# Kernel tuning notes

Hardware: AMD Instinct MI355X
Metric: run time of the kernel (lower is better)

The kernel has to match this reference:

```python
import jax, jax.numpy as jnp
import numpy as np

N_NODES = 30000
N_EDGES = 300000
NUM_GRAPHS = 512
HID = 600
IN_FEATS = 9
NUM_TASKS = 128


def setup_inputs() -> dict:
    key = jax.random.key(0)
    ks = jax.random.split(key, 20)
    s = 0.05  # small init scale to keep activations bounded over 5 layers
    inp = {
        'x': jax.random.normal(ks[0], (N_NODES, IN_FEATS), jnp.float32),
        'edge_index': jax.random.randint(ks[1], (2, N_EDGES), 0, N_NODES, jnp.int64),
        'batch_ind': jnp.sort(jax.random.randint(ks[2], (N_NODES,), 0, NUM_GRAPHS, jnp.int64)),
        'w1_0': jax.random.normal(ks[3], (IN_FEATS, HID), jnp.float32) * s,
        'b1_0': jax.random.normal(ks[4], (HID,), jnp.float32) * s,
        'w2_0': jax.random.normal(ks[5], (HID, HID), jnp.float32) * s,
        'b2_0': jax.random.normal(ks[6], (HID,), jnp.float32) * s,
        'w1_r': jax.random.normal(ks[7], (4, HID, HID), jnp.float32) * s,
        'b1_r': jax.random.normal(ks[8], (4, HID), jnp.float32) * s,
        'w2_r': jax.random.normal(ks[9], (4, HID, HID), jnp.float32) * s,
        'b2_r': jax.random.normal(ks[10], (4, HID), jnp.float32) * s,
        'cw1': jax.random.normal(ks[11], (HID, 256), jnp.float32) * s,
        'cb1': jax.random.normal(ks[12], (256,), jnp.float32) * s,
        'cw2': jax.random.normal(ks[13], (256, 256), jnp.float32) * s,
        'cb2': jax.random.normal(ks[14], (256,), jnp.float32) * s,
        'cw3': jax.random.normal(ks[15], (256, NUM_TASKS), jnp.float32) * s,
        'cb3': jax.random.normal(ks[16], (NUM_TASKS,), jnp.float32) * s,
    }
    return inp


def _gin_conv(h, edge_index, w1, b1, w2, b2):
    # sum-aggregate neighbor features: messages flow src -> dst
    msgs = h[edge_index[0]]                                   # [E, d] gather
    agg = jax.ops.segment_sum(msgs, edge_index[1], num_segments=N_NODES)
    z = h + agg                                               # (1 + eps) * x + agg, eps = 0
    z = jax.nn.relu(z @ w1 + b1) @ w2 + b2                    # per-layer MLP [in, 600, 600]
    return z


def _forward(x, edge_index, batch_ind, w1_0, b1_0, w2_0, b2_0,
             w1_r, b1_r, w2_r, b2_r, cw1, cb1, cw2, cb2, cw3, cb3):
    h = _gin_conv(x, edge_index, w1_0, b1_0, w2_0, b2_0)
    h = jax.nn.relu(h)  # inter-layer activation (dropout is identity in eval)
    for i in range(4):  # layers 1..4 (fixed, structurally distinct params)
        h = _gin_conv(h, edge_index, w1_r[i], b1_r[i], w2_r[i], b2_r[i])
        if i < 3:
            h = jax.nn.relu(h)  # no act/dropout after final GNN layer (jk=None)
    feats = jax.ops.segment_sum(h, batch_ind, num_segments=NUM_GRAPHS)  # global_add_pool
    z = jax.nn.relu(feats @ cw1 + cb1)
    z = jax.nn.relu(z @ cw2 + cb2)
    return z @ cw3 + cb3  # [NUM_GRAPHS, NUM_TASKS]


def reference(x, edge_index, batch_ind, w1_0, b1_0, w2_0, b2_0,
              w1_r, b1_r, w2_r, b2_r, cw1, cb1, cw2, cb2, cw3, cb3):
    return _forward(x, edge_index, batch_ind, w1_0, b1_0, w2_0, b2_0,
                    w1_r, b1_r, w2_r, b2_r, cw1, cb1, cw2, cb2, cw3, cb3)
```

## Files before the change

### kernel.cpp

```cpp
#include <hip/hip_runtime.h>

#define N_NODES 30000
#define N_EDGES 300000
#define NUM_GRAPHS 512
#define HID 600
#define IN_FEATS 9
#define NUM_TASKS 128

#define MPAD 30080
#define HPAD 640
#define K0PAD 32

typedef __attribute__((ext_vector_type(4))) float f32x4;
typedef __attribute__((ext_vector_type(8))) short bf16x8;


__device__ __forceinline__ float bflo(unsigned int v) {
  union { unsigned int u; float f; } c; c.u = v << 16; return c.f;
}
__device__ __forceinline__ float bfhi(unsigned int v) {
  union { unsigned int u; float f; } c; c.u = v & 0xffff0000u; return c.f;
}
__device__ __forceinline__ unsigned short f2bf(float f) {
  union { float f; unsigned int u; } c; c.f = f;
  unsigned int u = c.u;
  return (unsigned short)((u + 0x7fffu + ((u >> 16) & 1u)) >> 16);
}
__device__ __forceinline__ unsigned int pack2(float a, float b) {
  return (unsigned int)f2bf(a) | ((unsigned int)f2bf(b) << 16);
}


__global__ void k_hist(const int* __restrict__ keys, int* __restrict__ counts, int n) {
  int i = blockIdx.x * blockDim.x + threadIdx.x;
  if (i < n) atomicAdd(&counts[keys[i]], 1);
}

__global__ __launch_bounds__(1024) void k_exscan(const int* __restrict__ in,
                                                 int* __restrict__ out,
                                                 int* cursor, int n) {
  __shared__ int buf[1024];
  int tid = threadIdx.x;
  int CH = (n + 1023) / 1024;
  int base = tid * CH;
  int s = 0;
  for (int j = 0; j < CH; ++j) {
    int i = base + j;
    if (i < n) s += in[i];
  }
  buf[tid] = s;
  __syncthreads();
  for (int off = 1; off < 1024; off <<= 1) {
    int t = (tid >= off) ? buf[tid - off] : 0;
    __syncthreads();
    buf[tid] += t;
    __syncthreads();
  }
  int pre = (tid == 0) ? 0 : buf[tid - 1];
  for (int j = 0; j < CH; ++j) {
    int i = base + j;
    if (i <= n) out[i] = pre;
    if (i < n) {
      int v = in[i];
      if (cursor) cursor[i] = pre;
      pre += v;
    }
  }
}

__global__ __launch_bounds__(256) void k_scan1(const int* __restrict__ in,
                                               int* __restrict__ partials, int n) {
  __shared__ int buf[256];
  int i = blockIdx.x * 256 + threadIdx.x;
  buf[threadIdx.x] = (i < n) ? in[i] : 0;
  __syncthreads();
  for (int off = 128; off; off >>= 1) {
    if (threadIdx.x < off) buf[threadIdx.x] += buf[threadIdx.x + off];
    __syncthreads();
  }
  if (threadIdx.x == 0) partials[blockIdx.x] = buf[0];
}

__global__ __launch_bounds__(256) void k_scan3(const int* __restrict__ in,
                                               const int* __restrict__ poff,
                                               int* __restrict__ out,
                                               int* __restrict__ cursor, int n) {
  __shared__ int buf[256];
  int b = blockIdx.x, t = threadIdx.x;
  int i = b * 256 + t;
  int v = (i < n) ? in[i] : 0;
  buf[t] = v;
  __syncthreads();
  for (int off = 1; off < 256; off <<= 1) {
    int x = (t >= off) ? buf[t - off] : 0;
    __syncthreads();
    buf[t] += x;
    __syncthreads();
  }
  int base = poff[b];
  int excl = base + buf[t] - v;
  if (i < n) {
    out[i] = excl;
    cursor[i] = excl;
    if (i == n - 1) out[n] = base + buf[t];
  }
}

__global__ void k_scatter(const int* __restrict__ src, const int* __restrict__ dst,
                          int* __restrict__ cursor, int* __restrict__ edge_src, int E) {
  int e = blockIdx.x * blockDim.x + threadIdx.x;
  if (e < E) {
    int pos = atomicAdd(&cursor[dst[e]], 1);
    edge_src[pos] = src[e];
  }
}


__global__ void k_wt0(const float* __restrict__ w1_0, unsigned short* __restrict__ wt0) {
  int idx = blockIdx.x * 256 + threadIdx.x;
  if (idx >= HPAD * K0PAD) return;
  int n = idx / K0PAD, k = idx % K0PAD;
  float v = (n < HID && k < IN_FEATS) ? w1_0[(size_t)k * HID + n] : 0.f;
  wt0[idx] = f2bf(v);
}

__global__ __launch_bounds__(256) void k_wt_tiled(
    const float* __restrict__ w2_0, const float* __restrict__ w1_r,
    const float* __restrict__ w2_r, unsigned short* __restrict__ wts) {
  __shared__ float tile[64][65];
  int b = blockIdx.x;
  int w = b / 100;
  int tb = b % 100;
  int tn = (tb % 10) * 64;
  int tk = (tb / 10) * 64;
  const float* W;
  if (w == 0) W = w2_0;
  else if (w < 5) W = w1_r + (size_t)(w - 1) * HID * HID;
  else W = w2_r + (size_t)(w - 5) * HID * HID;
  int t = threadIdx.x;
  int lx = t & 63, ly = t >> 6;
#pragma unroll
  for (int i = 0; i < 16; ++i) {
    int k = tk + ly + i * 4;
    int n = tn + lx;
    float v = (k < HID && n < HID) ? W[(size_t)k * HID + n] : 0.f;
    tile[ly + i * 4][lx] = v;
  }
  __syncthreads();
  unsigned short* dst = wts + (size_t)w * HPAD * HPAD;
#pragma unroll
  for (int i = 0; i < 16; ++i) {
    int n = tn + ly + i * 4;
    int k = tk + lx;
    dst[(size_t)n * HPAD + k] = f2bf(tile[lx][ly + i * 4]);
  }
}

__global__ void k_bias_all(const float* __restrict__ b1_0, const float* __restrict__ b2_0,
                           const float* __restrict__ b1_r, const float* __restrict__ b2_r,
                           float* __restrict__ biases) {
  int idx = blockIdx.x * 256 + threadIdx.x;
  if (idx >= 10 * HPAD) return;
  int w = idx / HPAD, i = idx % HPAD;
  float v = 0.f;
  if (i < HID) {
    if (w == 0) v = b1_0[i];
    else if (w == 1) v = b2_0[i];
    else if (w < 6) v = b1_r[(size_t)(w - 2) * HID + i];
    else v = b2_r[(size_t)(w - 6) * HID + i];
  }
  biases[idx] = v;
}

__global__ void k_xconv(const float* __restrict__ x, unsigned short* __restrict__ xb) {
  int idx = blockIdx.x * 256 + threadIdx.x;
  if (idx >= MPAD * K0PAD) return;
  int m = idx >> 5, k = idx & 31;
  float v = (m < N_NODES && k < IN_FEATS) ? x[(size_t)m * IN_FEATS + k] : 0.f;
  xb[idx] = f2bf(v);
}


template <int U>
__global__ __launch_bounds__(256) void k_agg_bf16(
    const unsigned int* __restrict__ h, const int* __restrict__ ptr,
    const int* __restrict__ esrc, unsigned int* __restrict__ z, int n_nodes) {
  int wave = threadIdx.x >> 6, lane = threadIdx.x & 63;
  int node = blockIdx.x * 4 + wave;
  if (node >= n_nodes) return;
  int beg = ptr[node], end = ptr[node + 1];
  const unsigned int* hn = h + (size_t)node * U;
  float a0[5], a1[5];
#pragma unroll
  for (int i = 0; i < 5; ++i) {
    int u = lane + i * 64;
    if (u < U) { unsigned int v = hn[u]; a0[i] = bflo(v); a1[i] = bfhi(v); }
    else { a0[i] = 0.f; a1[i] = 0.f; }
  }
  int e = beg;
  for (; e + 4 <= end; e += 4) {
    const unsigned int* p0 = h + (size_t)esrc[e] * U;
    const unsigned int* p1 = h + (size_t)esrc[e + 1] * U;
    const unsigned int* p2 = h + (size_t)esrc[e + 2] * U;
    const unsigned int* p3 = h + (size_t)esrc[e + 3] * U;
    unsigned int v0[5], v1[5], v2[5], v3[5];
#pragma unroll
    for (int i = 0; i < 5; ++i) {
      int u = lane + i * 64;
      if (u < U) { v0[i] = p0[u]; v1[i] = p1[u]; v2[i] = p2[u]; v3[i] = p3[u]; }
      else { v0[i] = 0; v1[i] = 0; v2[i] = 0; v3[i] = 0; }
    }
#pragma unroll
    for (int i = 0; i < 5; ++i) {
      a0[i] += (bflo(v0[i]) + bflo(v1[i])) + (bflo(v2[i]) + bflo(v3[i]));
      a1[i] += (bfhi(v0[i]) + bfhi(v1[i])) + (bfhi(v2[i]) + bfhi(v3[i]));
    }
  }
  for (; e < end; ++e) {
    const unsigned int* p0 = h + (size_t)esrc[e] * U;
#pragma unroll
    for (int i = 0; i < 5; ++i) {
      int u = lane + i * 64;
      if (u < U) { unsigned int v = p0[u]; a0[i] += bflo(v); a1[i] += bfhi(v); }
    }
  }
  unsigned int* zn = z + (size_t)node * U;
#pragma unroll
  for (int i = 0; i < 5; ++i) {
    int u = lane + i * 64;
    if (u < U) zn[u] = pack2(a0[i], a1[i]);
  }
}


__global__ __launch_bounds__(256) void k_pool_bf16(
    const unsigned int* __restrict__ h, const int* __restrict__ gptr,
    float* __restrict__ feats) {
  const int U = HPAD / 2;
  __shared__ float red[4][HPAD];
  int t = threadIdx.x;
  int wave = t >> 6, lane = t & 63;
  int g = blockIdx.x;
  int beg = gptr[g], end = gptr[g + 1];
  float a0[5] = {0.f, 0.f, 0.f, 0.f, 0.f}, a1[5] = {0.f, 0.f, 0.f, 0.f, 0.f};
  for (int i = beg + wave; i < end; i += 4) {
    const unsigned int* hi = h + (size_t)i * U;
#pragma unroll
    for (int j = 0; j < 5; ++j) {
      unsigned int v = hi[lane + j * 64];
      a0[j] += bflo(v); a1[j] += bfhi(v);
    }
  }
#pragma unroll
  for (int j = 0; j < 5; ++j) {
    int u = lane + j * 64;
    red[wave][2 * u] = a0[j];
    red[wave][2 * u + 1] = a1[j];
  }
  __syncthreads();
  float* fg = feats + (size_t)g * HPAD;
  for (int c = t; c < HPAD; c += 256)
    fg[c] = red[0][c] + red[1][c] + red[2][c] + red[3][c];
}


#define GLOAD(gptr, lptr)                                                            \
  __builtin_amdgcn_global_load_lds(                                                  \
      (const __attribute__((address_space(1))) unsigned int*)(gptr),                 \
      (__attribute__((address_space(3))) unsigned int*)(lptr), 16, 0, 0)

__global__ __launch_bounds__(512, 6) void k_mgemm(
    const unsigned short* __restrict__ A, const unsigned short* __restrict__ Bt,
    const float* __restrict__ bias, unsigned short* __restrict__ C,
    int lda, int ldb, int ldc, int K, int relu, int gy) {
  int G = gridDim.x;
  int orig = blockIdx.x;
  int q = G >> 3, r = G & 7;
  int xcd = orig & 7, local = orig >> 3;
  int wgid = (xcd < r ? xcd * (q + 1) : r * (q + 1) + (xcd - r) * q) + local;
  int n0 = (wgid % gy) * 128;
  int m0 = (wgid / gy) * 128;

  __shared__ unsigned short smem[3 * 4096 * 2];
  unsigned short* Asb = smem;
  unsigned short* Bsb = smem + 12288;

  int t = threadIdx.x;
  int lane = t & 63, wave = t >> 6;
  int wm = (wave >> 2) * 64;
  int wn = (wave & 3) * 32;

  f32x4 acc[4][2] = {};

  int off = t * 8;
  int rm = off >> 5, rk = off & 31;

  const unsigned short* Ar = A + (size_t)(m0 + rm) * lda + rk;
  const unsigned short* Br = Bt + (size_t)(n0 + rm) * ldb + rk;

  int nt = K >> 5;
  GLOAD(Ar, Asb + off);
  GLOAD(Br, Bsb + off);
  if (nt > 1) {
    GLOAD(Ar + 32, Asb + 4096 + off);
    GLOAD(Br + 32, Bsb + 4096 + off);
  }

  int kk = (lane >> 4) * 8;
  int ra = wm + (lane & 15);
  int rb = wn + (lane & 15);
  int cur = 0;

  for (int tt = 0; tt < nt; ++tt) {
    if (tt + 1 < nt) {
      asm volatile("s_waitcnt vmcnt(2)" ::: "memory");
    } else {
      asm volatile("s_waitcnt vmcnt(0)" ::: "memory");
    }
    __builtin_amdgcn_s_barrier();
    if (tt + 2 < nt) {
      int k2 = (tt + 2) << 5;
      int nb = cur + 2; if (nb >= 3) nb -= 3;
      GLOAD(Ar + k2, Asb + nb * 4096 + off);
      GLOAD(Br + k2, Bsb + nb * 4096 + off);
    }
    bf16x8 a[4], b[2];
#pragma unroll
    for (int i = 0; i < 4; ++i)
      a[i] = *(const bf16x8*)(Asb + cur * 4096 + (ra + i * 16) * 32 + kk);
#pragma unroll
    for (int j = 0; j < 2; ++j)
      b[j] = *(const bf16x8*)(Bsb + cur * 4096 + (rb + j * 16) * 32 + kk);
#pragma unroll
    for (int i = 0; i < 4; ++i)
#pragma unroll
      for (int j = 0; j < 2; ++j)
        acc[i][j] = __builtin_amdgcn_mfma_f32_16x16x32_bf16(b[j], a[i], acc[i][j], 0, 0, 0);
    cur += 1; if (cur >= 3) cur = 0;
  }

  __syncthreads();
  int colm = lane & 15;
  int nq = (lane >> 4) * 4;
#pragma unroll
  for (int j = 0; j < 2; ++j) {
    int nloc = wn + j * 16 + nq;
    f32x4 bv = *(const f32x4*)&bias[n0 + nloc];
#pragma unroll
    for (int i = 0; i < 4; ++i) {
      int mloc = wm + i * 16 + colm;
      float v0 = acc[i][j][0] + bv[0];
      float v1 = acc[i][j][1] + bv[1];
      float v2 = acc[i][j][2] + bv[2];
      float v3 = acc[i][j][3] + bv[3];
      if (relu) {
        v0 = fmaxf(v0, 0.f); v1 = fmaxf(v1, 0.f);
        v2 = fmaxf(v2, 0.f); v3 = fmaxf(v3, 0.f);
      }
      uint2 w;
      w.x = pack2(v0, v1);
      w.y = pack2(v2, v3);
      int nblk = (nloc >> 2) ^ ((mloc & 7) << 2);
      *(uint2*)&smem[mloc * 128 + nblk * 4] = w;
    }
  }
  __syncthreads();
#pragma unroll
  for (int p = 0; p < 4; ++p) {
    int idx = p * 4096 + t * 8;
    int mloc = idx >> 7;
    int ncol = idx & 127;
    int s = (mloc & 7) << 2;
    int nb0 = (ncol >> 2) ^ s;
    int nb1 = ((ncol >> 2) + 1) ^ s;
    uint2 w0 = *(uint2*)&smem[mloc * 128 + nb0 * 4];
    uint2 w1 = *(uint2*)&smem[mloc * 128 + nb1 * 4];
    uint4 w;
    w.x = w0.x; w.y = w0.y; w.z = w1.x; w.w = w1.y;
    *(uint4*)&C[(size_t)(m0 + mloc) * ldc + n0 + ncol] = w;
  }
}


__global__ __launch_bounds__(256) void k_classifier(
    const float* __restrict__ feats,
    const float* __restrict__ cw1, const float* __restrict__ cb1,
    const float* __restrict__ cw2, const float* __restrict__ cb2,
    const float* __restrict__ cw3, const float* __restrict__ cb3,
    float* __restrict__ out) {
  __shared__ float f[HID];
  __shared__ float red[4][256];
  __shared__ float z1[256];
  __shared__ float z2[256];
  int g = blockIdx.x;
  int t = threadIdx.x;
  int wave = t >> 6, lane = t & 63;
  for (int i = t; i < HID; i += 256) f[i] = feats[(size_t)g * HPAD + i];
  __syncthreads();

  {
    float acc[4] = {0.f, 0.f, 0.f, 0.f};
    int k0 = wave * 150, k1 = k0 + 150;
    for (int k = k0; k < k1; ++k) {
      float fv = f[k];
      const float* row = cw1 + (size_t)k * 256;
#pragma unroll
      for (int j = 0; j < 4; ++j) acc[j] += fv * row[lane + j * 64];
    }
#pragma unroll
    for (int j = 0; j < 4; ++j) red[wave][lane + j * 64] = acc[j];
  }
  __syncthreads();
  z1[t] = fmaxf(red[0][t] + red[1][t] + red[2][t] + red[3][t] + cb1[t], 0.f);
  __syncthreads();

  {
    float acc[4] = {0.f, 0.f, 0.f, 0.f};
    int k0 = wave * 64, k1 = k0 + 64;
    for (int k = k0; k < k1; ++k) {
      float zv = z1[k];
      const float* row = cw2 + (size_t)k * 256;
#pragma unroll
      for (int j = 0; j < 4; ++j) acc[j] += zv * row[lane + j * 64];
    }
    __syncthreads();
#pragma unroll
    for (int j = 0; j < 4; ++j) red[wave][lane + j * 64] = acc[j];
  }
  __syncthreads();
  z2[t] = fmaxf(red[0][t] + red[1][t] + red[2][t] + red[3][t] + cb2[t], 0.f);
  __syncthreads();

  {
    float a0 = 0.f, a1 = 0.f;
    int k0 = wave * 64, k1 = k0 + 64;
    for (int k = k0; k < k1; ++k) {
      float zv = z2[k];
      const float* row = cw3 + (size_t)k * NUM_TASKS;
      a0 += zv * row[lane];
      a1 += zv * row[lane + 64];
    }
    __syncthreads();
    red[wave][lane] = a0;
    red[wave][lane + 64] = a1;
  }
  __syncthreads();
  if (t < NUM_TASKS)
    out[(size_t)g * NUM_TASKS + t] = red[0][t] + red[1][t] + red[2][t] + red[3][t] + cb3[t];
}


extern "C" void kernel_launch(void* const* d_in, const int* in_sizes, int n_in,
                              void* d_out, int out_size, void* d_ws, size_t ws_size,
                              hipStream_t stream) {
  const float* x      = (const float*)d_in[0];
  const int*   ei     = (const int*)d_in[1];
  const int*   batch  = (const int*)d_in[2];
  const float* w1_0   = (const float*)d_in[3];
  const float* b1_0   = (const float*)d_in[4];
  const float* w2_0   = (const float*)d_in[5];
  const float* b2_0   = (const float*)d_in[6];
  const float* w1_r   = (const float*)d_in[7];
  const float* b1_r   = (const float*)d_in[8];
  const float* w2_r   = (const float*)d_in[9];
  const float* b2_r   = (const float*)d_in[10];
  const float* cw1    = (const float*)d_in[11];
  const float* cb1    = (const float*)d_in[12];
  const float* cw2    = (const float*)d_in[13];
  const float* cb2    = (const float*)d_in[14];
  const float* cw3    = (const float*)d_in[15];
  const float* cb3    = (const float*)d_in[16];
  float* out = (float*)d_out;

  const int* e_src = ei;
  const int* e_dst = ei + N_EDGES;

  const size_t HBUF = (size_t)MPAD * HPAD;
  const size_t ZBUF = (size_t)MPAD * K0PAD;
  const size_t WT   = (size_t)HPAD * HPAD;
  const int NB = (N_NODES + 255) / 256;

  unsigned short* hA  = (unsigned short*)d_ws;
  unsigned short* hB  = hA + HBUF;
  unsigned short* hC  = hB + HBUF;
  unsigned short* z0  = hC + HBUF;
  unsigned short* xb  = z0 + ZBUF;
  unsigned short* wt0 = xb + ZBUF;
  unsigned short* wts = wt0 + (size_t)HPAD * K0PAD;
  float* biases = (float*)(wts + 9 * WT);
  float* feats  = biases + 10 * HPAD;
  int* row_ptr  = (int*)(feats + (size_t)NUM_GRAPHS * HPAD);
  int* counts   = row_ptr + (N_NODES + 1);
  int* edge_src = counts + N_NODES;
  int* gptr     = edge_src + N_EDGES;
  int* gcnt     = gptr + (NUM_GRAPHS + 1);
  int* partials = gcnt + NUM_GRAPHS;
  int* poff     = partials + (NB + 1);

  k_wt0<<<(HPAD * K0PAD + 255) / 256, 256, 0, stream>>>(w1_0, wt0);
  k_wt_tiled<<<9 * 100, 256, 0, stream>>>(w2_0, w1_r, w2_r, wts);
  k_bias_all<<<(10 * HPAD + 255) / 256, 256, 0, stream>>>(b1_0, b2_0, b1_r, b2_r, biases);
  k_xconv<<<(MPAD * K0PAD + 255) / 256, 256, 0, stream>>>(x, xb);

  hipMemsetAsync(counts, 0, N_NODES * sizeof(int), stream);
  k_hist<<<(N_EDGES + 255) / 256, 256, 0, stream>>>(e_dst, counts, N_EDGES);
  k_scan1<<<NB, 256, 0, stream>>>(counts, partials, N_NODES);
  k_exscan<<<1, 1024, 0, stream>>>(partials, poff, nullptr, NB);
  k_scan3<<<NB, 256, 0, stream>>>(counts, poff, row_ptr, counts, N_NODES);
  k_scatter<<<(N_EDGES + 255) / 256, 256, 0, stream>>>(e_src, e_dst, counts, edge_src, N_EDGES);

  hipMemsetAsync(gcnt, 0, NUM_GRAPHS * sizeof(int), stream);
  k_hist<<<(N_NODES + 255) / 256, 256, 0, stream>>>(batch, gcnt, N_NODES);
  k_exscan<<<1, 1024, 0, stream>>>(gcnt, gptr, nullptr, NUM_GRAPHS);

  const int G = (MPAD / 128) * (HPAD / 128);
  const int GY = HPAD / 128;

  k_agg_bf16<K0PAD / 2><<<(N_NODES + 3) / 4, 256, 0, stream>>>(
      (const unsigned int*)xb, row_ptr, edge_src, (unsigned int*)z0, N_NODES);
  k_mgemm<<<G, 512, 0, stream>>>(z0, wt0, biases + 0 * HPAD, hC, K0PAD, K0PAD, HPAD, K0PAD, 1, GY);
  k_mgemm<<<G, 512, 0, stream>>>(hC, wts, biases + 1 * HPAD, hA, HPAD, HPAD, HPAD, HPAD, 1, GY);

  unsigned short* h = hA;
  unsigned short* z = hB;
  unsigned short* tb = hC;
  for (int i = 0; i < 4; ++i) {
    k_agg_bf16<HPAD / 2><<<(N_NODES + 3) / 4, 256, 0, stream>>>(
        (const unsigned int*)h, row_ptr, edge_src, (unsigned int*)z, N_NODES);
    k_mgemm<<<G, 512, 0, stream>>>(z, wts + (1 + (size_t)i) * WT, biases + (2 + i) * HPAD, tb,
                                   HPAD, HPAD, HPAD, HPAD, 1, GY);
    k_mgemm<<<G, 512, 0, stream>>>(tb, wts + (5 + (size_t)i) * WT, biases + (6 + i) * HPAD, z,
                                   HPAD, HPAD, HPAD, HPAD, (i < 3) ? 1 : 0, GY);
    unsigned short* tmp = h; h = z; z = tmp;
  }

  k_pool_bf16<<<NUM_GRAPHS, 256, 0, stream>>>((const unsigned int*)h, gptr, feats);
  k_classifier<<<NUM_GRAPHS, 256, 0, stream>>>(feats, cw1, cb1, cw2, cb2, cw3, cb3, out);
}
```

Measured before the change: 720.9 us.

## Fuse setup kernels, merge pool with classifier, add LDS swizzle GEMM variant

Several small preprocessing kernels (weight transpose for layer 0, bias packing, x conversion, both histograms) are merged into one launch. Pooling is folded into the classifier kernel, which removes the feats buffer round trip. A templated GEMM adds an XOR swizzle on the LDS k-offset to reduce bank conflicts, but it is only used for the last two layers, which looks like an A/B experiment. MPAD also grows to 30208, adding a little padded work in exchange for launch and memory-traffic savings.

```diff
diff --git a/kernel.cpp b/kernel.cpp
--- a/kernel.cpp
+++ b/kernel.cpp
@@ -7,7 +7,7 @@
 #define IN_FEATS 9
 #define NUM_TASKS 128
 
-#define MPAD 30080
+#define MPAD 30208
 #define HPAD 640
 #define K0PAD 32
 
@@ -31,10 +31,56 @@
 }
 
 
-__global__ void k_hist(const int* __restrict__ keys, int* __restrict__ counts, int n) {
-  int i = blockIdx.x * blockDim.x + threadIdx.x;
-  if (i < n) atomicAdd(&counts[keys[i]], 1);
-}
+__global__ void k_setup(const float* __restrict__ w1_0,
+                        const float* __restrict__ b1_0, const float* __restrict__ b2_0,
+                        const float* __restrict__ b1_r, const float* __restrict__ b2_r,
+                        const float* __restrict__ x,
+                        const int* __restrict__ e_dst, const int* __restrict__ batch,
+                        unsigned short* __restrict__ wt0, float* __restrict__ biases,
+                        unsigned short* __restrict__ xb,
+                        int* __restrict__ counts, int* __restrict__ gcnt) {
+  const int S0 = HPAD * K0PAD;
+  const int S1 = 10 * HPAD;
+  const int S2 = MPAD * K0PAD;
+  const int S3 = N_EDGES;
+  int idx = blockIdx.x * 256 + threadIdx.x;
+  if (idx < S0) {
+    int n = idx / K0PAD, k = idx % K0PAD;
+    float v = (n < HID && k < IN_FEATS) ? w1_0[(size_t)k * HID + n] : 0.f;
+    wt0[idx] = f2bf(v);
+    return;
+  }
+  idx -= S0;
+  if (idx < S1) {
+    int w = idx / HPAD, i = idx % HPAD;
+    float v = 0.f;
+    if (i < HID) {
+      if (w == 0) v = b1_0[i];
+      else if (w == 1) v = b2_0[i];
+      else if (w < 6) v = b1_r[(size_t)(w - 2) * HID + i];
+      else v = b2_r[(size_t)(w - 6) * HID + i];
+    }
+    biases[idx] = v;
+    return;
+  }
+  idx -= S1;
+  if (idx < S2) {
+    int m = idx >> 5, k = idx & 31;
+    float v = (m < N_NODES && k < IN_FEATS) ? x[(size_t)m * IN_FEATS + k] : 0.f;
+    xb[idx] = f2bf(v);
+    return;
+  }
+  idx -= S2;
+  if (idx < S3) {
+    atomicAdd(&counts[e_dst[idx]], 1);
+    return;
+  }
+  idx -= S3;
+  if (idx < N_NODES) {
+    atomicAdd(&gcnt[batch[idx]], 1);
+  }
+}
+
 
 __global__ __launch_bounds__(1024) void k_exscan(const int* __restrict__ in,
                                                  int* __restrict__ out,
@@ -115,14 +161,6 @@
   }
 }
 
-
-__global__ void k_wt0(const float* __restrict__ w1_0, unsigned short* __restrict__ wt0) {
-  int idx = blockIdx.x * 256 + threadIdx.x;
-  if (idx >= HPAD * K0PAD) return;
-  int n = idx / K0PAD, k = idx % K0PAD;
-  float v = (n < HID && k < IN_FEATS) ? w1_0[(size_t)k * HID + n] : 0.f;
-  wt0[idx] = f2bf(v);
-}
 
 __global__ __launch_bounds__(256) void k_wt_tiled(
     const float* __restrict__ w2_0, const float* __restrict__ w1_r,
@@ -156,30 +194,6 @@
   }
 }
 
-__global__ void k_bias_all(const float* __restrict__ b1_0, const float* __restrict__ b2_0,
-                           const float* __restrict__ b1_r, const float* __restrict__ b2_r,
-                           float* __restrict__ biases) {
-  int idx = blockIdx.x * 256 + threadIdx.x;
-  if (idx >= 10 * HPAD) return;
-  int w = idx / HPAD, i = idx % HPAD;
-  float v = 0.f;
-  if (i < HID) {
-    if (w == 0) v = b1_0[i];
-    else if (w == 1) v = b2_0[i];
-    else if (w < 6) v = b1_r[(size_t)(w - 2) * HID + i];
-    else v = b2_r[(size_t)(w - 6) * HID + i];
-  }
-  biases[idx] = v;
-}
-
-__global__ void k_xconv(const float* __restrict__ x, unsigned short* __restrict__ xb) {
-  int idx = blockIdx.x * 256 + threadIdx.x;
-  if (idx >= MPAD * K0PAD) return;
-  int m = idx >> 5, k = idx & 31;
-  float v = (m < N_NODES && k < IN_FEATS) ? x[(size_t)m * IN_FEATS + k] : 0.f;
-  xb[idx] = f2bf(v);
-}
-
 
 template <int U>
 __global__ __launch_bounds__(256) void k_agg_bf16(
@@ -233,43 +247,13 @@
 }
 
 
-__global__ __launch_bounds__(256) void k_pool_bf16(
-    const unsigned int* __restrict__ h, const int* __restrict__ gptr,
-    float* __restrict__ feats) {
-  const int U = HPAD / 2;
-  __shared__ float red[4][HPAD];
-  int t = threadIdx.x;
-  int wave = t >> 6, lane = t & 63;
-  int g = blockIdx.x;
-  int beg = gptr[g], end = gptr[g + 1];
-  float a0[5] = {0.f, 0.f, 0.f, 0.f, 0.f}, a1[5] = {0.f, 0.f, 0.f, 0.f, 0.f};
-  for (int i = beg + wave; i < end; i += 4) {
-    const unsigned int* hi = h + (size_t)i * U;
-#pragma unroll
-    for (int j = 0; j < 5; ++j) {
-      unsigned int v = hi[lane + j * 64];
-      a0[j] += bflo(v); a1[j] += bfhi(v);
-    }
-  }
-#pragma unroll
-  for (int j = 0; j < 5; ++j) {
-    int u = lane + j * 64;
-    red[wave][2 * u] = a0[j];
-    red[wave][2 * u + 1] = a1[j];
-  }
-  __syncthreads();
-  float* fg = feats + (size_t)g * HPAD;
-  for (int c = t; c < HPAD; c += 256)
-    fg[c] = red[0][c] + red[1][c] + red[2][c] + red[3][c];
-}
-
-
 #define GLOAD(gptr, lptr)                                                            \
   __builtin_amdgcn_global_load_lds(                                                  \
       (const __attribute__((address_space(1))) unsigned int*)(gptr),                 \
       (__attribute__((address_space(3))) unsigned int*)(lptr), 16, 0, 0)
 
-__global__ __launch_bounds__(512, 6) void k_mgemm(
+template <int SWZ>
+__global__ __launch_bounds__(512, 6) void k_mgemm_t(
     const unsigned short* __restrict__ A, const unsigned short* __restrict__ Bt,
     const float* __restrict__ bias, unsigned short* __restrict__ C,
     int lda, int ldb, int ldc, int K, int relu, int gy) {
@@ -294,9 +278,10 @@
 
   int off = t * 8;
   int rm = off >> 5, rk = off & 31;
-
-  const unsigned short* Ar = A + (size_t)(m0 + rm) * lda + rk;
-  const unsigned short* Br = Bt + (size_t)(n0 + rm) * ldb + rk;
+  int rksrc = SWZ ? ((((rk >> 3) ^ (rm & 3)) & 3) << 3) : rk;
+
+  const unsigned short* Ar = A + (size_t)(m0 + rm) * lda + rksrc;
+  const unsigned short* Br = Bt + (size_t)(n0 + rm) * ldb + rksrc;
 
   int nt = K >> 5;
   GLOAD(Ar, Asb + off);
@@ -306,9 +291,11 @@
     GLOAD(Br + 32, Bsb + 4096 + off);
   }
 
-  int kk = (lane >> 4) * 8;
+  int qq = lane >> 4;
   int ra = wm + (lane & 15);
   int rb = wn + (lane & 15);
+  int kka = SWZ ? ((qq ^ (ra & 3)) << 3) : (qq << 3);
+  int kkb = SWZ ? ((qq ^ (rb & 3)) << 3) : (qq << 3);
   int cur = 0;
 
   for (int tt = 0; tt < nt; ++tt) {
@@ -327,10 +314,10 @@
     bf16x8 a[4], b[2];
 #pragma unroll
     for (int i = 0; i < 4; ++i)
-      a[i] = *(const bf16x8*)(Asb + cur * 4096 + (ra + i * 16) * 32 + kk);
+      a[i] = *(const bf16x8*)(Asb + cur * 4096 + (ra + i * 16) * 32 + kka);
 #pragma unroll
     for (int j = 0; j < 2; ++j)
-      b[j] = *(const bf16x8*)(Bsb + cur * 4096 + (rb + j * 16) * 32 + kk);
+      b[j] = *(const bf16x8*)(Bsb + cur * 4096 + (rb + j * 16) * 32 + kkb);
 #pragma unroll
     for (int i = 0; i < 4; ++i)
 #pragma unroll
@@ -382,20 +369,43 @@
 }
 
 
-__global__ __launch_bounds__(256) void k_classifier(
-    const float* __restrict__ feats,
+__global__ __launch_bounds__(256) void k_poolcls(
+    const unsigned int* __restrict__ h, const int* __restrict__ gptr,
     const float* __restrict__ cw1, const float* __restrict__ cb1,
     const float* __restrict__ cw2, const float* __restrict__ cb2,
     const float* __restrict__ cw3, const float* __restrict__ cb3,
     float* __restrict__ out) {
-  __shared__ float f[HID];
-  __shared__ float red[4][256];
+  const int U = HPAD / 2;
+  __shared__ float red[4][HPAD];
+  __shared__ float f[HPAD];
+  __shared__ float red2[4][256];
   __shared__ float z1[256];
   __shared__ float z2[256];
   int g = blockIdx.x;
   int t = threadIdx.x;
   int wave = t >> 6, lane = t & 63;
-  for (int i = t; i < HID; i += 256) f[i] = feats[(size_t)g * HPAD + i];
+  int beg = gptr[g], end = gptr[g + 1];
+
+  {
+    float a0[5] = {0.f, 0.f, 0.f, 0.f, 0.f}, a1[5] = {0.f, 0.f, 0.f, 0.f, 0.f};
+    for (int i = beg + wave; i < end; i += 4) {
+      const unsigned int* hi = h + (size_t)i * U;
+#pragma unroll
+      for (int j = 0; j < 5; ++j) {
+        unsigned int v = hi[lane + j * 64];
+        a0[j] += bflo(v); a1[j] += bfhi(v);
+      }
+    }
+#pragma unroll
+    for (int j = 0; j < 5; ++j) {
+      int u = lane + j * 64;
+      red[wave][2 * u] = a0[j];
+      red[wave][2 * u + 1] = a1[j];
+    }
+  }
+  __syncthreads();
+  for (int c = t; c < HPAD; c += 256)
+    f[c] = red[0][c] + red[1][c] + red[2][c] + red[3][c];
   __syncthreads();
 
   {
@@ -408,10 +418,10 @@
       for (int j = 0; j < 4; ++j) acc[j] += fv * row[lane + j * 64];
     }
 #pragma unroll
-    for (int j = 0; j < 4; ++j) red[wave][lane + j * 64] = acc[j];
-  }
-  __syncthreads();
-  z1[t] = fmaxf(red[0][t] + red[1][t] + red[2][t] + red[3][t] + cb1[t], 0.f);
+    for (int j = 0; j < 4; ++j) red2[wave][lane + j * 64] = acc[j];
+  }
+  __syncthreads();
+  z1[t] = fmaxf(red2[0][t] + red2[1][t] + red2[2][t] + red2[3][t] + cb1[t], 0.f);
   __syncthreads();
 
   {
@@ -425,10 +435,10 @@
     }
     __syncthreads();
 #pragma unroll
-    for (int j = 0; j < 4; ++j) red[wave][lane + j * 64] = acc[j];
-  }
-  __syncthreads();
-  z2[t] = fmaxf(red[0][t] + red[1][t] + red[2][t] + red[3][t] + cb2[t], 0.f);
+    for (int j = 0; j < 4; ++j) red2[wave][lane + j * 64] = acc[j];
+  }
+  __syncthreads();
+  z2[t] = fmaxf(red2[0][t] + red2[1][t] + red2[2][t] + red2[3][t] + cb2[t], 0.f);
   __syncthreads();
 
   {
@@ -441,12 +451,12 @@
       a1 += zv * row[lane + 64];
     }
     __syncthreads();
-    red[wave][lane] = a0;
-    red[wave][lane + 64] = a1;
+    red2[wave][lane] = a0;
+    red2[wave][lane + 64] = a1;
   }
   __syncthreads();
   if (t < NUM_TASKS)
-    out[(size_t)g * NUM_TASKS + t] = red[0][t] + red[1][t] + red[2][t] + red[3][t] + cb3[t];
+    out[(size_t)g * NUM_TASKS + t] = red2[0][t] + red2[1][t] + red2[2][t] + red2[3][t] + cb3[t];
 }
 
 
@@ -488,8 +498,7 @@
   unsigned short* wt0 = xb + ZBUF;
   unsigned short* wts = wt0 + (size_t)HPAD * K0PAD;
   float* biases = (float*)(wts + 9 * WT);
-  float* feats  = biases + 10 * HPAD;
-  int* row_ptr  = (int*)(feats + (size_t)NUM_GRAPHS * HPAD);
+  int* row_ptr  = (int*)(biases + 10 * HPAD);
   int* counts   = row_ptr + (N_NODES + 1);
   int* edge_src = counts + N_NODES;
   int* gptr     = edge_src + N_EDGES;
@@ -497,29 +506,28 @@
   int* partials = gcnt + NUM_GRAPHS;
   int* poff     = partials + (NB + 1);
 
-  k_wt0<<<(HPAD * K0PAD + 255) / 256, 256, 0, stream>>>(w1_0, wt0);
+  hipMemsetAsync(counts, 0, N_NODES * sizeof(int), stream);
+  hipMemsetAsync(gcnt, 0, NUM_GRAPHS * sizeof(int), stream);
+  {
+    int total = HPAD * K0PAD + 10 * HPAD + MPAD * K0PAD + N_EDGES + N_NODES;
+    k_setup<<<(total + 255) / 256, 256, 0, stream>>>(
+        w1_0, b1_0, b2_0, b1_r, b2_r, x, e_dst, batch, wt0, biases, xb, counts, gcnt);
+  }
   k_wt_tiled<<<9 * 100, 256, 0, stream>>>(w2_0, w1_r, w2_r, wts);
-  k_bias_all<<<(10 * HPAD + 255) / 256, 256, 0, stream>>>(b1_0, b2_0, b1_r, b2_r, biases);
-  k_xconv<<<(MPAD * K0PAD + 255) / 256, 256, 0, stream>>>(x, xb);
-
-  hipMemsetAsync(counts, 0, N_NODES * sizeof(int), stream);
-  k_hist<<<(N_EDGES + 255) / 256, 256, 0, stream>>>(e_dst, counts, N_EDGES);
+
   k_scan1<<<NB, 256, 0, stream>>>(counts, partials, N_NODES);
   k_exscan<<<1, 1024, 0, stream>>>(partials, poff, nullptr, NB);
   k_scan3<<<NB, 256, 0, stream>>>(counts, poff, row_ptr, counts, N_NODES);
   k_scatter<<<(N_EDGES + 255) / 256, 256, 0, stream>>>(e_src, e_dst, counts, edge_src, N_EDGES);
-
-  hipMemsetAsync(gcnt, 0, NUM_GRAPHS * sizeof(int), stream);
-  k_hist<<<(N_NODES + 255) / 256, 256, 0, stream>>>(batch, gcnt, N_NODES);
   k_exscan<<<1, 1024, 0, stream>>>(gcnt, gptr, nullptr, NUM_GRAPHS);
 
-  const int G = (MPAD / 128) * (HPAD / 128);
+  const int G16 = (MPAD / 128) * (HPAD / 128);
   const int GY = HPAD / 128;
 
   k_agg_bf16<K0PAD / 2><<<(N_NODES + 3) / 4, 256, 0, stream>>>(
       (const unsigned int*)xb, row_ptr, edge_src, (unsigned int*)z0, N_NODES);
-  k_mgemm<<<G, 512, 0, stream>>>(z0, wt0, biases + 0 * HPAD, hC, K0PAD, K0PAD, HPAD, K0PAD, 1, GY);
-  k_mgemm<<<G, 512, 0, stream>>>(hC, wts, biases + 1 * HPAD, hA, HPAD, HPAD, HPAD, HPAD, 1, GY);
+  k_mgemm_t<0><<<G16, 512, 0, stream>>>(z0, wt0, biases + 0 * HPAD, hC, K0PAD, K0PAD, HPAD, K0PAD, 1, GY);
+  k_mgemm_t<0><<<G16, 512, 0, stream>>>(hC, wts, biases + 1 * HPAD, hA, HPAD, HPAD, HPAD, HPAD, 1, GY);
 
   unsigned short* h = hA;
   unsigned short* z = hB;
@@ -527,13 +535,20 @@
   for (int i = 0; i < 4; ++i) {
     k_agg_bf16<HPAD / 2><<<(N_NODES + 3) / 4, 256, 0, stream>>>(
         (const unsigned int*)h, row_ptr, edge_src, (unsigned int*)z, N_NODES);
-    k_mgemm<<<G, 512, 0, stream>>>(z, wts + (1 + (size_t)i) * WT, biases + (2 + i) * HPAD, tb,
-                                   HPAD, HPAD, HPAD, HPAD, 1, GY);
-    k_mgemm<<<G, 512, 0, stream>>>(tb, wts + (5 + (size_t)i) * WT, biases + (6 + i) * HPAD, z,
-                                   HPAD, HPAD, HPAD, HPAD, (i < 3) ? 1 : 0, GY);
+    if (i < 2) {
+      k_mgemm_t<0><<<G16, 512, 0, stream>>>(z, wts + (1 + (size_t)i) * WT, biases + (2 + i) * HPAD, tb,
+                                            HPAD, HPAD, HPAD, HPAD, 1, GY);
+      k_mgemm_t<0><<<G16, 512, 0, stream>>>(tb, wts + (5 + (size_t)i) * WT, biases + (6 + i) * HPAD, z,
+                                            HPAD, HPAD, HPAD, HPAD, 1, GY);
+    } else {
+      k_mgemm_t<1><<<G16, 512, 0, stream>>>(z, wts + (1 + (size_t)i) * WT, biases + (2 + i) * HPAD, tb,
+                                            HPAD, HPAD, HPAD, HPAD, 1, GY);
+      k_mgemm_t<1><<<G16, 512, 0, stream>>>(tb, wts + (5 + (size_t)i) * WT, biases + (6 + i) * HPAD, z,
+                                            HPAD, HPAD, HPAD, HPAD, (i < 3) ? 1 : 0, GY);
+    }
     unsigned short* tmp = h; h = z; z = tmp;
   }
 
-  k_pool_bf16<<<NUM_GRAPHS, 256, 0, stream>>>((const unsigned int*)h, gptr, feats);
-  k_classifier<<<NUM_GRAPHS, 256, 0, stream>>>(feats, cw1, cb1, cw2, cb2, cw3, cb3, out);
-}
+  k_poolcls<<<NUM_GRAPHS, 256, 0, stream>>>((const unsigned int*)h, gptr,
+                                            cw1, cb1, cw2, cb2, cw3, cb3, out);
+}
```

Result: no change. 709.9 us (-1.5%).
